# Performance work log

Measured on AMD Instinct MI355X. Metric: run time of the kernel, lower is better.

Reference implementation:

```python
import jax, jax.numpy as jnp
import numpy as np

D_MODEL = 512
N_HEADS = 8
HEAD_DIM = D_MODEL // N_HEADS
SEQ = 2048
BATCH = 2
EPS = 1e-5
SCALE = 1.0 / np.sqrt(HEAD_DIM).astype(np.float32)
# (kind, window, dilation) per head, matching init_kwargs head_specs
SPECS = [("global", 0, 1), ("global", 0, 1),
         ("window", 64, 1), ("window", 128, 1), ("window", 256, 1),
         ("dilated", 64, 2), ("dilated", 64, 4), ("dilated", 64, 8)]


def build_masks(N):
    i = jnp.arange(N)
    D = jnp.abs(i[:, None] - i[None, :])
    ms = []
    for kind, w, dil in SPECS:
        if kind == "global":
            ms.append(jnp.ones((N, N), dtype=bool))
        elif kind == "window":
            ms.append(D <= w)
        else:  # dilated
            ms.append((D % dil == 0) & (D // dil <= w))
    return jnp.stack(ms)  # [H, N, N] bool


def layernorm(x, g, b):
    mu = jnp.mean(x, axis=-1, keepdims=True)
    var = jnp.mean((x - mu) ** 2, axis=-1, keepdims=True)
    return (x - mu) * jax.lax.rsqrt(var + EPS) * g + b


def setup_inputs() -> dict:
    key = jax.random.key(0)
    ks = jax.random.split(key, 7)
    w = 0.02
    return {
        "x": jax.random.normal(ks[0], (BATCH, SEQ, D_MODEL), dtype=jnp.float32),
        "Wq": jax.random.normal(ks[1], (D_MODEL, D_MODEL), dtype=jnp.float32) * w,
        "Wk": jax.random.normal(ks[2], (D_MODEL, D_MODEL), dtype=jnp.float32) * w,
        "Wv": jax.random.normal(ks[3], (D_MODEL, D_MODEL), dtype=jnp.float32) * w,
        "Wo": jax.random.normal(ks[4], (D_MODEL, D_MODEL), dtype=jnp.float32) * w,
        "T_w1": jax.random.normal(ks[5], (D_MODEL, D_MODEL), dtype=jnp.float32) * w,
        "T_b1": jnp.zeros((D_MODEL,), dtype=jnp.float32),
        "T_w2": jax.random.normal(ks[6], (1, D_MODEL), dtype=jnp.float32) * w,
        "T_b2": jnp.zeros((1,), dtype=jnp.float32),
        "ln_in_g": jnp.ones((D_MODEL,), dtype=jnp.float32),
        "ln_in_b": jnp.zeros((D_MODEL,), dtype=jnp.float32),
        "ln_out_g": jnp.ones((D_MODEL,), dtype=jnp.float32),
        "ln_out_b": jnp.zeros((D_MODEL,), dtype=jnp.float32),
    }


def reference(x, Wq, Wk, Wv, Wo, T_w1, T_b1, T_w2, T_b2,
              ln_in_g, ln_in_b, ln_out_g, ln_out_b):
    B, N, H = x.shape
    x0 = x
    xn = layernorm(x, ln_in_g, ln_in_b)
    # torch Linear: y = x @ W.T ; reshape to [B, h, N, d]
    def heads(W):
        return (xn @ W.T).reshape(B, N, N_HEADS, HEAD_DIM).transpose(0, 2, 1, 3)
    Q, K, V = heads(Wq), heads(Wk), heads(Wv)
    attn = jnp.einsum("bhqd,bhkd->bhqk", Q, K) * SCALE
    mask = build_masks(N)  # [h, N, N]
    attn = jnp.where(mask[None], attn, -jnp.inf)
    attn = jax.nn.softmax(attn, axis=-1)  # every row has diagonal unmasked
    out = jnp.einsum("bhqk,bhkd->bhqd", attn, V)
    out = out.transpose(0, 2, 1, 3).reshape(B, N, N_HEADS * HEAD_DIM)
    out = out @ Wo.T
    # tanh-gated softmax over sequence dim
    T_logits = jnp.tanh(xn @ T_w1.T + T_b1) @ T_w2.T + T_b2  # [B, N, 1]
    T = jax.nn.softmax(T_logits, axis=1)
    out = out * T
    return layernorm(out + x0, ln_out_g, ln_out_b)
```

## Files before the change

### kernel.cpp

```cpp
#include <hip/hip_runtime.h>
#include <math.h>

#define N_SEQ 2048
#define DM    512
#define NTOK  4096
#define NH    8
#define HD    64
#define NSLOT 25
#define CHUNK 5

typedef __attribute__((ext_vector_type(8))) short short8;
typedef __attribute__((ext_vector_type(4))) short short4_t;
typedef __attribute__((ext_vector_type(4))) float f32x4;

__device__ inline short f2bf(float x) {
    union { float f; unsigned u; } v; v.f = x;
    unsigned r = v.u + 0x7fff + ((v.u >> 16) & 1);
    return (short)(r >> 16);
}
__device__ inline float bf2f(short s) {
    union { unsigned u; float f; } v; v.u = ((unsigned)(unsigned short)s) << 16;
    return v.f;
}
__device__ inline unsigned pkbf(float a, float b) {
    return ((unsigned)(unsigned short)f2bf(b) << 16) | (unsigned)(unsigned short)f2bf(a);
}
__device__ inline float ftanh(float x) {
    float e = __expf(2.f * x);
    return 1.f - 2.f / (e + 1.f);
}

__device__ inline f32x4 mfma16(short8 a, short8 b, f32x4 c) {
    return __builtin_amdgcn_mfma_f32_16x16x32_bf16(a, b, c, 0, 0, 0);
}

__device__ __forceinline__ void async_cp16(const short* g, short* l) {
    __builtin_amdgcn_global_load_lds(
        (const __attribute__((address_space(1))) void*)g,
        (__attribute__((address_space(3))) void*)l, 16, 0, 0);
}

__global__ __launch_bounds__(128) void k_ln(const float* __restrict__ x,
                                            const float* __restrict__ g,
                                            const float* __restrict__ b,
                                            short* __restrict__ y,
                                            float* __restrict__ lg) {
    int tk = blockIdx.x, t = threadIdx.x;
    if (t == 0) lg[tk] = 0.f;
    float4 xv = ((const float4*)(x + (size_t)tk * DM))[t];
    float s = xv.x + xv.y + xv.z + xv.w;
    float q = xv.x*xv.x + xv.y*xv.y + xv.z*xv.z + xv.w*xv.w;
    for (int o = 32; o; o >>= 1) { s += __shfl_down(s, o); q += __shfl_down(q, o); }
    __shared__ float ls[2], lq[2];
    if ((t & 63) == 0) { ls[t >> 6] = s; lq[t >> 6] = q; }
    __syncthreads();
    s = ls[0] + ls[1]; q = lq[0] + lq[1];
    float mu = s * (1.f / DM);
    float var = q * (1.f / DM) - mu * mu;
    float rs = rsqrtf(var + 1e-5f);
    float4 gv = ((const float4*)g)[t], bv = ((const float4*)b)[t];
    short4_t o;
    o[0] = f2bf((xv.x - mu) * rs * gv.x + bv.x);
    o[1] = f2bf((xv.y - mu) * rs * gv.y + bv.y);
    o[2] = f2bf((xv.z - mu) * rs * gv.z + bv.z);
    o[3] = f2bf((xv.w - mu) * rs * gv.w + bv.w);
    *(short4_t*)&y[(size_t)tk * DM + t * 4] = o;
}

__global__ __launch_bounds__(256) void k_cvtw(
    const float* __restrict__ Wq, const float* __restrict__ Wk,
    const float* __restrict__ Wv, const float* __restrict__ Tw1,
    const float* __restrict__ Wo,
    short* __restrict__ wcat, short* __restrict__ wo) {
    int id = blockIdx.x * 256 + threadIdx.x;
    if (id < 262144) {
        int z = id >> 16; int off = id & 65535;
        const float* s = (z == 0) ? Wq : (z == 1) ? Wk : (z == 2) ? Wv : Tw1;
        float4 v = ((const float4*)s)[off];
        short4_t o = {f2bf(v.x), f2bf(v.y), f2bf(v.z), f2bf(v.w)};
        *(short4_t*)(wcat + (size_t)z * 262144 + (size_t)off * 4) = o;
    } else {
        int off = id - 262144;
        float4 v = ((const float4*)Wo)[off];
        short4_t o = {f2bf(v.x), f2bf(v.y), f2bf(v.z), f2bf(v.w)};
        *(short4_t*)(wo + (size_t)off * 4) = o;
    }
}

__global__ __launch_bounds__(256) void k_gemm(
    const short* __restrict__ A, const short* __restrict__ W, int qkvt,
    const float* __restrict__ Tb1, const float* __restrict__ Tw2,
    short* __restrict__ qb, short* __restrict__ kb, short* __restrict__ vb,
    float* __restrict__ lg, float* __restrict__ proj) {
    __shared__ short As[128 * 32];
    __shared__ short Bs[128 * 32];
    int t = threadIdx.x;
    int lane = t & 63, w = t >> 6;
    int wy = w >> 1, wx = w & 1;
    int ln = lane & 15, q4 = lane >> 4;
    int c0 = blockIdx.x * 128, m0 = blockIdx.y * 128;
    int sr = t >> 2, sc = (t & 3) << 3;
    f32x4 acc[4][4];
    f32x4 zero = {0.f, 0.f, 0.f, 0.f};
    #pragma unroll
    for (int i = 0; i < 4; i++)
        #pragma unroll
        for (int j = 0; j < 4; j++) acc[i][j] = zero;
    for (int k0 = 0; k0 < DM; k0 += 32) {
        __syncthreads();
        async_cp16(&A[(size_t)(m0 + sr) * DM + k0 + sc],      &As[sr * 32 + sc]);
        async_cp16(&A[(size_t)(m0 + 64 + sr) * DM + k0 + sc], &As[(64 + sr) * 32 + sc]);
        async_cp16(&W[(size_t)(c0 + sr) * DM + k0 + sc],      &Bs[sr * 32 + sc]);
        async_cp16(&W[(size_t)(c0 + 64 + sr) * DM + k0 + sc], &Bs[(64 + sr) * 32 + sc]);
        __syncthreads();
        short8 af[4], bfr[4];
        #pragma unroll
        for (int i = 0; i < 4; i++)
            af[i] = *(short8*)&As[(wy * 64 + i * 16 + ln) * 32 + q4 * 8];
        #pragma unroll
        for (int j = 0; j < 4; j++)
            bfr[j] = *(short8*)&Bs[(wx * 64 + j * 16 + ln) * 32 + q4 * 8];
        #pragma unroll
        for (int i = 0; i < 4; i++)
            #pragma unroll
            for (int j = 0; j < 4; j++)
                acc[i][j] = mfma16(af[i], bfr[j], acc[i][j]);
    }
    if (qkvt) {
        int z = c0 >> 9;
        if (z < 3) {
            short* dst = (z == 0) ? qb : (z == 1) ? kb : vb;
            float sc2 = (z == 0) ? 0.125f : 1.0f;
            #pragma unroll
            for (int i = 0; i < 4; i++)
                #pragma unroll
                for (int j = 0; j < 4; j++)
                    #pragma unroll
                    for (int r = 0; r < 4; r++) {
                        int row = m0 + wy * 64 + i * 16 + q4 * 4 + r;
                        int col = c0 + wx * 64 + j * 16 + ln;
                        int nin = col & 511;
                        int h = nin >> 6, d = nin & 63;
                        int bi = row >> 11, n = row & (N_SEQ - 1);
                        dst[(((size_t)bi * NH + h) * N_SEQ + n) * HD + d] =
                            f2bf(acc[i][j][r] * sc2);
                    }
        } else {
            #pragma unroll
            for (int i = 0; i < 4; i++) {
                #pragma unroll
                for (int r = 0; r < 4; r++) {
                    float s = 0.f;
                    #pragma unroll
                    for (int j = 0; j < 4; j++) {
                        int tc = (c0 & 511) + wx * 64 + j * 16 + ln;
                        s += ftanh(acc[i][j][r] + Tb1[tc]) * Tw2[tc];
                    }
                    s += __shfl_xor(s, 1);
                    s += __shfl_xor(s, 2);
                    s += __shfl_xor(s, 4);
                    s += __shfl_xor(s, 8);
                    if (ln == 0) {
                        int row = m0 + wy * 64 + i * 16 + q4 * 4 + r;
                        atomicAdd(&lg[row], s);
                    }
                }
            }
        }
    } else {
        #pragma unroll
        for (int i = 0; i < 4; i++)
            #pragma unroll
            for (int j = 0; j < 4; j++)
                #pragma unroll
                for (int r = 0; r < 4; r++) {
                    int row = m0 + wy * 64 + i * 16 + q4 * 4 + r;
                    int col = c0 + wx * 64 + j * 16 + ln;
                    proj[(size_t)row * DM + col] = acc[i][j][r];
                }
    }
}

__global__ __launch_bounds__(256) void k_vtr(const short* __restrict__ vb,
                                             short* __restrict__ vtb) {
    __shared__ short tile[64][80];
    int t = threadIdx.x;
    int n0 = blockIdx.x * 64, bh = blockIdx.y;
    const short* src = vb + (size_t)bh * N_SEQ * HD;
    short* dst = vtb + (size_t)bh * HD * N_SEQ;
    #pragma unroll
    for (int i = 0; i < 2; i++) {
        int id = t + 256 * i;
        int r = id >> 3, c = id & 7;
        *(short8*)&tile[r][c * 8] = *(const short8*)&src[(size_t)(n0 + r) * HD + c * 8];
    }
    __syncthreads();
    #pragma unroll
    for (int i = 0; i < 2; i++) {
        int id = t + 256 * i;
        int d = id >> 3, c = id & 7;
        short8 v;
        #pragma unroll
        for (int j = 0; j < 8; j++) v[j] = tile[c * 8 + j][d];
        *(short8*)&dst[(size_t)d * N_SEQ + n0 + c * 8] = v;
    }
}

__global__ __launch_bounds__(1024) void k_gate(const float* __restrict__ lg,
                                               float* __restrict__ gate) {
    int b = blockIdx.x, t = threadIdx.x;
    __shared__ float red[16];
    float v0 = lg[b * N_SEQ + t], v1 = lg[b * N_SEQ + 1024 + t];
    float m = fmaxf(v0, v1);
    for (int o = 32; o; o >>= 1) m = fmaxf(m, __shfl_down(m, o));
    if ((t & 63) == 0) red[t >> 6] = m;
    __syncthreads();
    if (t < 64) {
        float x = (t < 16) ? red[t] : -INFINITY;
        for (int o = 8; o; o >>= 1) x = fmaxf(x, __shfl_down(x, o));
        if (t == 0) red[0] = x;
    }
    __syncthreads();
    float M = red[0];
    float e0 = __expf(v0 - M), e1 = __expf(v1 - M);
    float s = e0 + e1;
    __syncthreads();
    for (int o = 32; o; o >>= 1) s += __shfl_down(s, o);
    if ((t & 63) == 0) red[t >> 6] = s;
    __syncthreads();
    if (t < 64) {
        float x = (t < 16) ? red[t] : 0.f;
        for (int o = 8; o; o >>= 1) x += __shfl_down(x, o);
        if (t == 0) red[0] = x;
    }
    __syncthreads();
    float inv = 1.f / red[0];
    gate[b * N_SEQ + t] = e0 * inv;
    gate[b * N_SEQ + 1024 + t] = e1 * inv;
}

__global__ __launch_bounds__(256) void k_attn(const short* __restrict__ qb,
                                              const short* __restrict__ kb,
                                              const short* __restrict__ vtb,
                                              short* __restrict__ P_O,
                                              float* __restrict__ P_ml) {
    __shared__ short Ks[64 * 72];
    __shared__ short Vt[64 * 72];
    __shared__ short Pa[4][16 * 72];
    int t = threadIdx.x;
    int lane = t & 63, w = t >> 6;
    int ln = lane & 15, q4 = lane >> 4;
    int slot = blockIdx.x, qt = blockIdx.y, bi = blockIdx.z;
    int q0 = qt * 64;
    int h, c;
    if (slot < 7)        { h = 0; c = slot; }
    else if (slot < 14)  { h = 1; c = slot - 7; }
    else if (slot == 14) { h = 2; c = 0; }
    else if (slot == 15) { h = 3; c = 0; }
    else if (slot < 18)  { h = 4; c = slot - 16; }
    else if (slot == 18) { h = 5; c = 0; }
    else if (slot < 21)  { h = 6; c = slot - 19; }
    else                 { h = 7; c = slot - 21; }
    int kind = (h < 2) ? 0 : (h < 5) ? 1 : 2;
    int wnd = (h == 2 || h >= 5) ? 64 : (h == 3) ? 128 : (h == 4) ? 256 : 0;
    int dsh = (h == 5) ? 1 : (h == 6) ? 2 : (h == 7) ? 3 : 0;
    int dmask = (1 << dsh) - 1;
    int wmax = (kind == 0) ? 0 : (wnd << dsh);
    int tLoU, tHiU;
    if (kind == 0) { tLoU = 0; tHiU = 31; }
    else { tLoU = (q0 - wmax) >> 6; tHiU = (q0 + 63 + wmax) >> 6; }
    int ktLo = tLoU + c * CHUNK;
    int ktHi = ktLo + CHUNK - 1;
    if (ktHi > tHiU) ktHi = tHiU;
    if (ktHi > 31) ktHi = 31;
    if (ktLo < 0) ktLo = 0;
    int p4 = (bi * 32 + qt) * NSLOT + slot;
    float* ml = P_ml + (size_t)p4 * 128;
    if (ktLo > ktHi) {
        if (t < 64) { ml[t] = -1e30f; ml[64 + t] = 0.f; }
        return;
    }
    const size_t base = ((size_t)bi * NH + h) * N_SEQ * HD;
    const short* Q = qb + base;
    const short* K = kb + base;
    const short* Vg = vtb + base;
    short8 qa[2];
    {
        const short* qrow = Q + (size_t)(q0 + w * 16 + ln) * HD + q4 * 8;
        qa[0] = *(const short8*)qrow;
        qa[1] = *(const short8*)(qrow + 32);
    }
    int qi = q0 + w * 16 + ln;
    float m_i = -1e30f, l_i = 0.f;
    f32x4 OT[4];
    f32x4 zero = {0.f, 0.f, 0.f, 0.f};
    #pragma unroll
    for (int d = 0; d < 4; d++) OT[d] = zero;
    short* Paw = Pa[w];
    for (int kt = ktLo; kt <= ktHi; kt++) {
        int k0 = kt << 6;
        __syncthreads();
        #pragma unroll
        for (int i2 = 0; i2 < 2; i2++) {
            int id = t + 256 * i2;
            int r = id >> 3, cc = id & 7;
            *(short8*)&Ks[r * 72 + cc * 8] =
                *(const short8*)&K[(size_t)(k0 + r) * HD + cc * 8];
            *(short8*)&Vt[r * 72 + cc * 8] =
                *(const short8*)&Vg[(size_t)r * N_SEQ + k0 + cc * 8];
        }
        __syncthreads();
        f32x4 ST[4];
        #pragma unroll
        for (int nt = 0; nt < 4; nt++) ST[nt] = zero;
        #pragma unroll
        for (int nt = 0; nt < 4; nt++) {
            #pragma unroll
            for (int ks = 0; ks < 2; ks++) {
                short8 af = *(short8*)&Ks[(nt * 16 + ln) * 72 + ks * 32 + q4 * 8];
                ST[nt] = mfma16(af, qa[ks], ST[nt]);
            }
        }
        if (kind != 0) {
            #pragma unroll
            for (int nt = 0; nt < 4; nt++)
                #pragma unroll
                for (int r = 0; r < 4; r++) {
                    int key = k0 + nt * 16 + q4 * 4 + r;
                    int dlt = qi - key; dlt = (dlt < 0) ? -dlt : dlt;
                    int valid;
                    if (kind == 1) valid = (dlt <= wnd);
                    else valid = ((dlt & dmask) == 0) && ((dlt >> dsh) <= wnd);
                    if (!valid) ST[nt][r] = -1e30f;
                }
        }
        float rm = -1e30f;
        #pragma unroll
        for (int nt = 0; nt < 4; nt++) {
            float a = fmaxf(ST[nt][0], ST[nt][1]);
            float b = fmaxf(ST[nt][2], ST[nt][3]);
            rm = fmaxf(rm, fmaxf(a, b));
        }
        rm = fmaxf(rm, __shfl_xor(rm, 16));
        rm = fmaxf(rm, __shfl_xor(rm, 32));
        float mn = fmaxf(m_i, rm);
        float sc = __expf(m_i - mn);
        float rs = 0.f;
        #pragma unroll
        for (int nt = 0; nt < 4; nt++) {
            float p0 = __expf(ST[nt][0] - mn);
            float p1 = __expf(ST[nt][1] - mn);
            float p2 = __expf(ST[nt][2] - mn);
            float p3 = __expf(ST[nt][3] - mn);
            rs += (p0 + p1) + (p2 + p3);
            *(unsigned*)&Paw[ln * 72 + nt * 16 + q4 * 4]     = pkbf(p0, p1);
            *(unsigned*)&Paw[ln * 72 + nt * 16 + q4 * 4 + 2] = pkbf(p2, p3);
        }
        rs += __shfl_xor(rs, 16);
        rs += __shfl_xor(rs, 32);
        l_i = l_i * sc + rs;
        m_i = mn;
        #pragma unroll
        for (int d = 0; d < 4; d++) OT[d] *= sc;
        short8 pb0 = *(short8*)&Paw[ln * 72 + q4 * 8];
        short8 pb1 = *(short8*)&Paw[ln * 72 + 32 + q4 * 8];
        #pragma unroll
        for (int dt = 0; dt < 4; dt++) {
            short8 a0 = *(short8*)&Vt[(dt * 16 + ln) * 72 + q4 * 8];
            short8 a1 = *(short8*)&Vt[(dt * 16 + ln) * 72 + 32 + q4 * 8];
            OT[dt] = mfma16(a0, pb0, OT[dt]);
            OT[dt] = mfma16(a1, pb1, OT[dt]);
        }
    }
    if (q4 == 0) { ml[w * 16 + ln] = m_i; ml[64 + w * 16 + ln] = l_i; }
    #pragma unroll
    for (int dt = 0; dt < 4; dt++) {
        *(unsigned*)&Paw[ln * 72 + dt * 16 + q4 * 4]     = pkbf(OT[dt][0], OT[dt][1]);
        *(unsigned*)&Paw[ln * 72 + dt * 16 + q4 * 4 + 2] = pkbf(OT[dt][2], OT[dt][3]);
    }
    short8 o0 = *(short8*)&Paw[ln * 72 + q4 * 16];
    short8 o1 = *(short8*)&Paw[ln * 72 + q4 * 16 + 8];
    short* Op = P_O + (size_t)p4 * 4096;
    *(short8*)&Op[(w * 16 + ln) * 64 + q4 * 16] = o0;
    *(short8*)&Op[(w * 16 + ln) * 64 + q4 * 16 + 8] = o1;
}

__global__ __launch_bounds__(256) void k_combine(const short* __restrict__ P_O,
                                                 const float* __restrict__ P_ml,
                                                 short* __restrict__ ob) {
    const int hbase[8] = {0, 7, 14, 15, 16, 18, 19, 21};
    const int hcnt[8]  = {7, 7, 1, 1, 2, 1, 2, 4};
    int h = blockIdx.x, qt = blockIdx.y, bi = blockIdx.z;
    int t = threadIdx.x;
    int row = t >> 2, c0 = (t & 3) * 16;
    int pb = (bi * 32 + qt) * NSLOT + hbase[h];
    int cnt = hcnt[h];
    float m = -1e30f;
    for (int s = 0; s < cnt; s++)
        m = fmaxf(m, P_ml[(size_t)(pb + s) * 128 + row]);
    float l = 0.f;
    float acc[16];
    #pragma unroll
    for (int j = 0; j < 16; j++) acc[j] = 0.f;
    for (int s = 0; s < cnt; s++) {
        float ms = P_ml[(size_t)(pb + s) * 128 + row];
        float ls = P_ml[(size_t)(pb + s) * 128 + 64 + row];
        if (ls > 0.f) {
            float sc = __expf(ms - m);
            l += ls * sc;
            const short* Op = P_O + (size_t)(pb + s) * 4096 + row * 64 + c0;
            short8 v0 = *(const short8*)Op;
            short8 v1 = *(const short8*)(Op + 8);
            #pragma unroll
            for (int j = 0; j < 8; j++) acc[j]     += bf2f(v0[j]) * sc;
            #pragma unroll
            for (int j = 0; j < 8; j++) acc[8 + j] += bf2f(v1[j]) * sc;
        }
    }
    float inv = 1.f / l;
    int n = qt * 64 + row;
    short8 o0, o1;
    #pragma unroll
    for (int j = 0; j < 8; j++) o0[j] = f2bf(acc[j] * inv);
    #pragma unroll
    for (int j = 0; j < 8; j++) o1[j] = f2bf(acc[8 + j] * inv);
    short* dst = ob + ((size_t)bi * N_SEQ + n) * DM + h * 64 + c0;
    *(short8*)dst = o0;
    *(short8*)(dst + 8) = o1;
}

__global__ __launch_bounds__(128) void k_final(const float* __restrict__ proj,
                                               const float* __restrict__ gate,
                                               const float* __restrict__ x0,
                                               const float* __restrict__ g,
                                               const float* __restrict__ b,
                                               float* __restrict__ out) {
    int tk = blockIdx.x, t = threadIdx.x;
    float gt = gate[tk];
    float4 pv = ((const float4*)(proj + (size_t)tk * DM))[t];
    float4 xv = ((const float4*)(x0 + (size_t)tk * DM))[t];
    float4 y;
    y.x = pv.x * gt + xv.x;
    y.y = pv.y * gt + xv.y;
    y.z = pv.z * gt + xv.z;
    y.w = pv.w * gt + xv.w;
    float s = y.x + y.y + y.z + y.w;
    float q = y.x*y.x + y.y*y.y + y.z*y.z + y.w*y.w;
    for (int o = 32; o; o >>= 1) { s += __shfl_down(s, o); q += __shfl_down(q, o); }
    __shared__ float ls[2], lq[2];
    if ((t & 63) == 0) { ls[t >> 6] = s; lq[t >> 6] = q; }
    __syncthreads();
    s = ls[0] + ls[1]; q = lq[0] + lq[1];
    float mu = s * (1.f / DM);
    float var = q * (1.f / DM) - mu * mu;
    float rs = rsqrtf(var + 1e-5f);
    float4 gv = ((const float4*)g)[t], bv = ((const float4*)b)[t];
    float4 o;
    o.x = (y.x - mu) * rs * gv.x + bv.x;
    o.y = (y.y - mu) * rs * gv.y + bv.y;
    o.z = (y.z - mu) * rs * gv.z + bv.z;
    o.w = (y.w - mu) * rs * gv.w + bv.w;
    ((float4*)(out + (size_t)tk * DM))[t] = o;
}

extern "C" void kernel_launch(void* const* d_in, const int* in_sizes, int n_in,
                              void* d_out, int out_size, void* d_ws, size_t ws_size,
                              hipStream_t stream) {
    (void)in_sizes; (void)n_in; (void)out_size; (void)ws_size;
    const float* x    = (const float*)d_in[0];
    const float* Wq   = (const float*)d_in[1];
    const float* Wk   = (const float*)d_in[2];
    const float* Wv   = (const float*)d_in[3];
    const float* Wo   = (const float*)d_in[4];
    const float* Tw1  = (const float*)d_in[5];
    const float* Tb1  = (const float*)d_in[6];
    const float* Tw2  = (const float*)d_in[7];
    const float* ling = (const float*)d_in[9];
    const float* linb = (const float*)d_in[10];
    const float* logg = (const float*)d_in[11];
    const float* logb = (const float*)d_in[12];
    float* out = (float*)d_out;

    const size_t SZ = (size_t)NTOK * DM;
    const int NPART = 2 * 32 * NSLOT;
    char* p = (char*)d_ws;
    short* xn   = (short*)p; p += SZ * 2;
    short* wcat = (short*)p; p += (size_t)2048 * DM * 2;
    short* wo   = (short*)p; p += (size_t)DM * DM * 2;
    short* qb   = (short*)p; p += SZ * 2;
    short* kb   = (short*)p; p += SZ * 2;
    short* vb   = (short*)p; p += SZ * 2;
    short* vtb  = (short*)p; p += SZ * 2;
    short* obuf = (short*)p; p += SZ * 2;
    float* lg   = (float*)p; p += (size_t)NTOK * 4;
    float* gate = (float*)p; p += (size_t)NTOK * 4;
    float* P_ml = (float*)p; p += (size_t)NPART * 128 * 4;
    float* proj = (float*)p;
    short* P_O  = (short*)p; p += (size_t)NPART * 4096 * 2;

    k_ln<<<NTOK, 128, 0, stream>>>(x, ling, linb, xn, lg);
    k_cvtw<<<1280, 256, 0, stream>>>(Wq, Wk, Wv, Tw1, Wo, wcat, wo);
    k_gemm<<<dim3(16, 32), 256, 0, stream>>>(xn, wcat, 1, Tb1, Tw2,
                                             qb, kb, vb, lg, nullptr);
    k_vtr<<<dim3(32, 16), 256, 0, stream>>>(vb, vtb);
    k_gate<<<2, 1024, 0, stream>>>(lg, gate);
    k_attn<<<dim3(NSLOT, 32, 2), 256, 0, stream>>>(qb, kb, vtb, P_O, P_ml);
    k_combine<<<dim3(8, 32, 2), 256, 0, stream>>>(P_O, P_ml, obuf);
    k_gemm<<<dim3(4, 32), 256, 0, stream>>>(obuf, wo, 0, nullptr, nullptr,
                                            nullptr, nullptr, nullptr, nullptr, proj);
    k_final<<<NTOK, 128, 0, stream>>>(proj, gate, x, logg, logb, out);
}
```

Baseline: 173.9 us.

## Merge small kernels, widen attention key tiles to 128, split output GEMM finer

Folds layernorm and weight conversion into one launch, and V transpose and gate softmax into another. The QKV/T GEMM and the output projection GEMM become separate kernels, and the output projection now uses 64-wide column tiles so it launches twice as many blocks. The attention kernel processes 128 keys per iteration instead of 64 and uses fewer partition slots (18 instead of 25), with the combine tables updated to match. The aim is to cut launch overhead and per-tile loop and sync overhead, at the cost of more LDS per attention block and less parallelism across slots.

```diff
diff --git a/kernel.cpp b/kernel.cpp
--- a/kernel.cpp
+++ b/kernel.cpp
@@ -6,8 +6,7 @@
 #define NTOK  4096
 #define NH    8
 #define HD    64
-#define NSLOT 25
-#define CHUNK 5
+#define NSLOT 18
 
 typedef __attribute__((ext_vector_type(8))) short short8;
 typedef __attribute__((ext_vector_type(4))) short short4_t;
@@ -40,58 +39,59 @@
         (__attribute__((address_space(3))) void*)l, 16, 0, 0);
 }
 
-__global__ __launch_bounds__(128) void k_ln(const float* __restrict__ x,
-                                            const float* __restrict__ g,
-                                            const float* __restrict__ b,
-                                            short* __restrict__ y,
-                                            float* __restrict__ lg) {
-    int tk = blockIdx.x, t = threadIdx.x;
-    if (t == 0) lg[tk] = 0.f;
-    float4 xv = ((const float4*)(x + (size_t)tk * DM))[t];
-    float s = xv.x + xv.y + xv.z + xv.w;
-    float q = xv.x*xv.x + xv.y*xv.y + xv.z*xv.z + xv.w*xv.w;
-    for (int o = 32; o; o >>= 1) { s += __shfl_down(s, o); q += __shfl_down(q, o); }
-    __shared__ float ls[2], lq[2];
-    if ((t & 63) == 0) { ls[t >> 6] = s; lq[t >> 6] = q; }
-    __syncthreads();
-    s = ls[0] + ls[1]; q = lq[0] + lq[1];
-    float mu = s * (1.f / DM);
-    float var = q * (1.f / DM) - mu * mu;
-    float rs = rsqrtf(var + 1e-5f);
-    float4 gv = ((const float4*)g)[t], bv = ((const float4*)b)[t];
-    short4_t o;
-    o[0] = f2bf((xv.x - mu) * rs * gv.x + bv.x);
-    o[1] = f2bf((xv.y - mu) * rs * gv.y + bv.y);
-    o[2] = f2bf((xv.z - mu) * rs * gv.z + bv.z);
-    o[3] = f2bf((xv.w - mu) * rs * gv.w + bv.w);
-    *(short4_t*)&y[(size_t)tk * DM + t * 4] = o;
-}
-
-__global__ __launch_bounds__(256) void k_cvtw(
+__global__ __launch_bounds__(256) void k_lncvt(
+    const float* __restrict__ x, const float* __restrict__ g,
+    const float* __restrict__ b, short* __restrict__ y, float* __restrict__ lg,
     const float* __restrict__ Wq, const float* __restrict__ Wk,
     const float* __restrict__ Wv, const float* __restrict__ Tw1,
     const float* __restrict__ Wo,
     short* __restrict__ wcat, short* __restrict__ wo) {
-    int id = blockIdx.x * 256 + threadIdx.x;
-    if (id < 262144) {
-        int z = id >> 16; int off = id & 65535;
-        const float* s = (z == 0) ? Wq : (z == 1) ? Wk : (z == 2) ? Wv : Tw1;
-        float4 v = ((const float4*)s)[off];
-        short4_t o = {f2bf(v.x), f2bf(v.y), f2bf(v.z), f2bf(v.w)};
-        *(short4_t*)(wcat + (size_t)z * 262144 + (size_t)off * 4) = o;
+    int blk = blockIdx.x, t = threadIdx.x;
+    if (blk < 2048) {
+        int sub = t >> 7, tt = t & 127;
+        int tk = blk * 2 + sub;
+        if (tt == 0) lg[tk] = 0.f;
+        float4 xv = ((const float4*)(x + (size_t)tk * DM))[tt];
+        float s = xv.x + xv.y + xv.z + xv.w;
+        float q = xv.x*xv.x + xv.y*xv.y + xv.z*xv.z + xv.w*xv.w;
+        for (int o = 32; o; o >>= 1) { s += __shfl_down(s, o); q += __shfl_down(q, o); }
+        __shared__ float ls[4], lq[4];
+        if ((t & 63) == 0) { ls[t >> 6] = s; lq[t >> 6] = q; }
+        __syncthreads();
+        s = ls[sub * 2] + ls[sub * 2 + 1];
+        q = lq[sub * 2] + lq[sub * 2 + 1];
+        float mu = s * (1.f / DM);
+        float var = q * (1.f / DM) - mu * mu;
+        float rs = rsqrtf(var + 1e-5f);
+        float4 gv = ((const float4*)g)[tt], bv = ((const float4*)b)[tt];
+        short4_t o;
+        o[0] = f2bf((xv.x - mu) * rs * gv.x + bv.x);
+        o[1] = f2bf((xv.y - mu) * rs * gv.y + bv.y);
+        o[2] = f2bf((xv.z - mu) * rs * gv.z + bv.z);
+        o[3] = f2bf((xv.w - mu) * rs * gv.w + bv.w);
+        *(short4_t*)&y[(size_t)tk * DM + tt * 4] = o;
     } else {
-        int off = id - 262144;
-        float4 v = ((const float4*)Wo)[off];
-        short4_t o = {f2bf(v.x), f2bf(v.y), f2bf(v.z), f2bf(v.w)};
-        *(short4_t*)(wo + (size_t)off * 4) = o;
-    }
-}
-
-__global__ __launch_bounds__(256) void k_gemm(
-    const short* __restrict__ A, const short* __restrict__ W, int qkvt,
+        int id = (blk - 2048) * 256 + t;
+        if (id < 262144) {
+            int z = id >> 16; int off = id & 65535;
+            const float* s = (z == 0) ? Wq : (z == 1) ? Wk : (z == 2) ? Wv : Tw1;
+            float4 v = ((const float4*)s)[off];
+            short4_t o = {f2bf(v.x), f2bf(v.y), f2bf(v.z), f2bf(v.w)};
+            *(short4_t*)(wcat + (size_t)z * 262144 + (size_t)off * 4) = o;
+        } else {
+            int off = id - 262144;
+            float4 v = ((const float4*)Wo)[off];
+            short4_t o = {f2bf(v.x), f2bf(v.y), f2bf(v.z), f2bf(v.w)};
+            *(short4_t*)(wo + (size_t)off * 4) = o;
+        }
+    }
+}
+
+__global__ __launch_bounds__(256) void k_gemmqkvt(
+    const short* __restrict__ A, const short* __restrict__ W,
     const float* __restrict__ Tb1, const float* __restrict__ Tw2,
     short* __restrict__ qb, short* __restrict__ kb, short* __restrict__ vb,
-    float* __restrict__ lg, float* __restrict__ proj) {
+    float* __restrict__ lg) {
     __shared__ short As[128 * 32];
     __shared__ short Bs[128 * 32];
     int t = threadIdx.x;
@@ -126,48 +126,10 @@
             for (int j = 0; j < 4; j++)
                 acc[i][j] = mfma16(af[i], bfr[j], acc[i][j]);
     }
-    if (qkvt) {
-        int z = c0 >> 9;
-        if (z < 3) {
-            short* dst = (z == 0) ? qb : (z == 1) ? kb : vb;
-            float sc2 = (z == 0) ? 0.125f : 1.0f;
-            #pragma unroll
-            for (int i = 0; i < 4; i++)
-                #pragma unroll
-                for (int j = 0; j < 4; j++)
-                    #pragma unroll
-                    for (int r = 0; r < 4; r++) {
-                        int row = m0 + wy * 64 + i * 16 + q4 * 4 + r;
-                        int col = c0 + wx * 64 + j * 16 + ln;
-                        int nin = col & 511;
-                        int h = nin >> 6, d = nin & 63;
-                        int bi = row >> 11, n = row & (N_SEQ - 1);
-                        dst[(((size_t)bi * NH + h) * N_SEQ + n) * HD + d] =
-                            f2bf(acc[i][j][r] * sc2);
-                    }
-        } else {
-            #pragma unroll
-            for (int i = 0; i < 4; i++) {
-                #pragma unroll
-                for (int r = 0; r < 4; r++) {
-                    float s = 0.f;
-                    #pragma unroll
-                    for (int j = 0; j < 4; j++) {
-                        int tc = (c0 & 511) + wx * 64 + j * 16 + ln;
-                        s += ftanh(acc[i][j][r] + Tb1[tc]) * Tw2[tc];
-                    }
-                    s += __shfl_xor(s, 1);
-                    s += __shfl_xor(s, 2);
-                    s += __shfl_xor(s, 4);
-                    s += __shfl_xor(s, 8);
-                    if (ln == 0) {
-                        int row = m0 + wy * 64 + i * 16 + q4 * 4 + r;
-                        atomicAdd(&lg[row], s);
-                    }
-                }
-            }
-        }
-    } else {
+    int z = c0 >> 9;
+    if (z < 3) {
+        short* dst = (z == 0) ? qb : (z == 1) ? kb : vb;
+        float sc2 = (z == 0) ? 0.125f : 1.0f;
         #pragma unroll
         for (int i = 0; i < 4; i++)
             #pragma unroll
@@ -176,67 +138,140 @@
                 for (int r = 0; r < 4; r++) {
                     int row = m0 + wy * 64 + i * 16 + q4 * 4 + r;
                     int col = c0 + wx * 64 + j * 16 + ln;
-                    proj[(size_t)row * DM + col] = acc[i][j][r];
+                    int nin = col & 511;
+                    int h = nin >> 6, d = nin & 63;
+                    int bi = row >> 11, n = row & (N_SEQ - 1);
+                    dst[(((size_t)bi * NH + h) * N_SEQ + n) * HD + d] =
+                        f2bf(acc[i][j][r] * sc2);
                 }
-    }
-}
-
-__global__ __launch_bounds__(256) void k_vtr(const short* __restrict__ vb,
-                                             short* __restrict__ vtb) {
+    } else {
+        #pragma unroll
+        for (int i = 0; i < 4; i++) {
+            #pragma unroll
+            for (int r = 0; r < 4; r++) {
+                float s = 0.f;
+                #pragma unroll
+                for (int j = 0; j < 4; j++) {
+                    int tc = (c0 & 511) + wx * 64 + j * 16 + ln;
+                    s += ftanh(acc[i][j][r] + Tb1[tc]) * Tw2[tc];
+                }
+                s += __shfl_xor(s, 1);
+                s += __shfl_xor(s, 2);
+                s += __shfl_xor(s, 4);
+                s += __shfl_xor(s, 8);
+                if (ln == 0) {
+                    int row = m0 + wy * 64 + i * 16 + q4 * 4 + r;
+                    atomicAdd(&lg[row], s);
+                }
+            }
+        }
+    }
+}
+
+__global__ __launch_bounds__(256) void k_gemmp(
+    const short* __restrict__ A, const short* __restrict__ W,
+    float* __restrict__ proj) {
+    __shared__ short As[128 * 32];
+    __shared__ short Bs[64 * 32];
+    int t = threadIdx.x;
+    int lane = t & 63, w = t >> 6;
+    int wy = w >> 1, wx = w & 1;
+    int ln = lane & 15, q4 = lane >> 4;
+    int c0 = blockIdx.x * 64, m0 = blockIdx.y * 128;
+    int sr = t >> 2, sc = (t & 3) << 3;
+    int br = t >> 2, bc = (t & 3) << 3;
+    f32x4 acc[4][2];
+    f32x4 zero = {0.f, 0.f, 0.f, 0.f};
+    #pragma unroll
+    for (int i = 0; i < 4; i++) { acc[i][0] = zero; acc[i][1] = zero; }
+    for (int k0 = 0; k0 < DM; k0 += 32) {
+        __syncthreads();
+        async_cp16(&A[(size_t)(m0 + sr) * DM + k0 + sc],      &As[sr * 32 + sc]);
+        async_cp16(&A[(size_t)(m0 + 64 + sr) * DM + k0 + sc], &As[(64 + sr) * 32 + sc]);
+        if (br < 64)
+            async_cp16(&W[(size_t)(c0 + br) * DM + k0 + bc], &Bs[br * 32 + bc]);
+        __syncthreads();
+        short8 af[4], bfr[2];
+        #pragma unroll
+        for (int i = 0; i < 4; i++)
+            af[i] = *(short8*)&As[(wy * 64 + i * 16 + ln) * 32 + q4 * 8];
+        #pragma unroll
+        for (int j = 0; j < 2; j++)
+            bfr[j] = *(short8*)&Bs[(wx * 32 + j * 16 + ln) * 32 + q4 * 8];
+        #pragma unroll
+        for (int i = 0; i < 4; i++)
+            #pragma unroll
+            for (int j = 0; j < 2; j++)
+                acc[i][j] = mfma16(af[i], bfr[j], acc[i][j]);
+    }
+    #pragma unroll
+    for (int i = 0; i < 4; i++)
+        #pragma unroll
+        for (int j = 0; j < 2; j++)
+            #pragma unroll
+            for (int r = 0; r < 4; r++) {
+                int row = m0 + wy * 64 + i * 16 + q4 * 4 + r;
+                int col = c0 + wx * 32 + j * 16 + ln;
+                proj[(size_t)row * DM + col] = acc[i][j][r];
+            }
+}
+
+__global__ __launch_bounds__(256) void k_vtrgate(const short* __restrict__ vb,
+                                                 short* __restrict__ vtb,
+                                                 const float* __restrict__ lg,
+                                                 float* __restrict__ gate) {
     __shared__ short tile[64][80];
-    int t = threadIdx.x;
-    int n0 = blockIdx.x * 64, bh = blockIdx.y;
-    const short* src = vb + (size_t)bh * N_SEQ * HD;
-    short* dst = vtb + (size_t)bh * HD * N_SEQ;
-    #pragma unroll
-    for (int i = 0; i < 2; i++) {
-        int id = t + 256 * i;
-        int r = id >> 3, c = id & 7;
-        *(short8*)&tile[r][c * 8] = *(const short8*)&src[(size_t)(n0 + r) * HD + c * 8];
-    }
-    __syncthreads();
-    #pragma unroll
-    for (int i = 0; i < 2; i++) {
-        int id = t + 256 * i;
-        int d = id >> 3, c = id & 7;
-        short8 v;
-        #pragma unroll
-        for (int j = 0; j < 8; j++) v[j] = tile[c * 8 + j][d];
-        *(short8*)&dst[(size_t)d * N_SEQ + n0 + c * 8] = v;
-    }
-}
-
-__global__ __launch_bounds__(1024) void k_gate(const float* __restrict__ lg,
-                                               float* __restrict__ gate) {
-    int b = blockIdx.x, t = threadIdx.x;
-    __shared__ float red[16];
-    float v0 = lg[b * N_SEQ + t], v1 = lg[b * N_SEQ + 1024 + t];
-    float m = fmaxf(v0, v1);
-    for (int o = 32; o; o >>= 1) m = fmaxf(m, __shfl_down(m, o));
-    if ((t & 63) == 0) red[t >> 6] = m;
-    __syncthreads();
-    if (t < 64) {
-        float x = (t < 16) ? red[t] : -INFINITY;
-        for (int o = 8; o; o >>= 1) x = fmaxf(x, __shfl_down(x, o));
-        if (t == 0) red[0] = x;
-    }
-    __syncthreads();
-    float M = red[0];
-    float e0 = __expf(v0 - M), e1 = __expf(v1 - M);
-    float s = e0 + e1;
-    __syncthreads();
-    for (int o = 32; o; o >>= 1) s += __shfl_down(s, o);
-    if ((t & 63) == 0) red[t >> 6] = s;
-    __syncthreads();
-    if (t < 64) {
-        float x = (t < 16) ? red[t] : 0.f;
-        for (int o = 8; o; o >>= 1) x += __shfl_down(x, o);
-        if (t == 0) red[0] = x;
-    }
-    __syncthreads();
-    float inv = 1.f / red[0];
-    gate[b * N_SEQ + t] = e0 * inv;
-    gate[b * N_SEQ + 1024 + t] = e1 * inv;
+    __shared__ float rg[8];
+    int blk = blockIdx.x, t = threadIdx.x;
+    if (blk < 512) {
+        int n0 = (blk & 31) * 64, bh = blk >> 5;
+        const short* src = vb + (size_t)bh * N_SEQ * HD;
+        short* dst = vtb + (size_t)bh * HD * N_SEQ;
+        #pragma unroll
+        for (int i = 0; i < 2; i++) {
+            int id = t + 256 * i;
+            int r = id >> 3, c = id & 7;
+            *(short8*)&tile[r][c * 8] = *(const short8*)&src[(size_t)(n0 + r) * HD + c * 8];
+        }
+        __syncthreads();
+        #pragma unroll
+        for (int i = 0; i < 2; i++) {
+            int id = t + 256 * i;
+            int d = id >> 3, c = id & 7;
+            short8 v;
+            #pragma unroll
+            for (int j = 0; j < 8; j++) v[j] = tile[c * 8 + j][d];
+            *(short8*)&dst[(size_t)d * N_SEQ + n0 + c * 8] = v;
+        }
+    } else {
+        int b = blk - 512;
+        float v[8];
+        {
+            float4 a0 = *(const float4*)&lg[b * N_SEQ + t * 8];
+            float4 a1 = *(const float4*)&lg[b * N_SEQ + t * 8 + 4];
+            v[0] = a0.x; v[1] = a0.y; v[2] = a0.z; v[3] = a0.w;
+            v[4] = a1.x; v[5] = a1.y; v[6] = a1.z; v[7] = a1.w;
+        }
+        float m = v[0];
+        #pragma unroll
+        for (int j = 1; j < 8; j++) m = fmaxf(m, v[j]);
+        for (int o = 32; o; o >>= 1) m = fmaxf(m, __shfl_down(m, o));
+        if ((t & 63) == 0) rg[t >> 6] = m;
+        __syncthreads();
+        m = fmaxf(fmaxf(rg[0], rg[1]), fmaxf(rg[2], rg[3]));
+        float e[8], s = 0.f;
+        #pragma unroll
+        for (int j = 0; j < 8; j++) { e[j] = __expf(v[j] - m); s += e[j]; }
+        for (int o = 32; o; o >>= 1) s += __shfl_down(s, o);
+        if ((t & 63) == 0) rg[4 + (t >> 6)] = s;
+        __syncthreads();
+        s = (rg[4] + rg[5]) + (rg[6] + rg[7]);
+        float inv = 1.f / s;
+        float4 o0 = {e[0] * inv, e[1] * inv, e[2] * inv, e[3] * inv};
+        float4 o1 = {e[4] * inv, e[5] * inv, e[6] * inv, e[7] * inv};
+        *(float4*)&gate[b * N_SEQ + t * 8] = o0;
+        *(float4*)&gate[b * N_SEQ + t * 8 + 4] = o1;
+    }
 }
 
 __global__ __launch_bounds__(256) void k_attn(const short* __restrict__ qb,
@@ -244,35 +279,35 @@
                                               const short* __restrict__ vtb,
                                               short* __restrict__ P_O,
                                               float* __restrict__ P_ml) {
-    __shared__ short Ks[64 * 72];
-    __shared__ short Vt[64 * 72];
-    __shared__ short Pa[4][16 * 72];
+    __shared__ short Ks[128 * 72];
+    __shared__ short Vt[64 * 136];
+    __shared__ short Pa[4][16 * 136];
     int t = threadIdx.x;
     int lane = t & 63, w = t >> 6;
     int ln = lane & 15, q4 = lane >> 4;
     int slot = blockIdx.x, qt = blockIdx.y, bi = blockIdx.z;
     int q0 = qt * 64;
     int h, c;
-    if (slot < 7)        { h = 0; c = slot; }
-    else if (slot < 14)  { h = 1; c = slot - 7; }
-    else if (slot == 14) { h = 2; c = 0; }
-    else if (slot == 15) { h = 3; c = 0; }
-    else if (slot < 18)  { h = 4; c = slot - 16; }
-    else if (slot == 18) { h = 5; c = 0; }
-    else if (slot < 21)  { h = 6; c = slot - 19; }
-    else                 { h = 7; c = slot - 21; }
+    if (slot < 4)        { h = 0; c = slot; }
+    else if (slot < 8)   { h = 1; c = slot - 4; }
+    else if (slot == 8)  { h = 2; c = 0; }
+    else if (slot == 9)  { h = 3; c = 0; }
+    else if (slot < 12)  { h = 4; c = slot - 10; }
+    else if (slot == 12) { h = 5; c = 0; }
+    else if (slot < 15)  { h = 6; c = slot - 13; }
+    else                 { h = 7; c = slot - 15; }
     int kind = (h < 2) ? 0 : (h < 5) ? 1 : 2;
     int wnd = (h == 2 || h >= 5) ? 64 : (h == 3) ? 128 : (h == 4) ? 256 : 0;
     int dsh = (h == 5) ? 1 : (h == 6) ? 2 : (h == 7) ? 3 : 0;
     int dmask = (1 << dsh) - 1;
     int wmax = (kind == 0) ? 0 : (wnd << dsh);
-    int tLoU, tHiU;
-    if (kind == 0) { tLoU = 0; tHiU = 31; }
-    else { tLoU = (q0 - wmax) >> 6; tHiU = (q0 + 63 + wmax) >> 6; }
-    int ktLo = tLoU + c * CHUNK;
-    int ktHi = ktLo + CHUNK - 1;
+    int tLoU, tHiU, CS;
+    if (kind == 0) { tLoU = 0; tHiU = 15; CS = 4; }
+    else { tLoU = (q0 - wmax) >> 7; tHiU = (q0 + 63 + wmax) >> 7; CS = 3; }
+    int ktLo = tLoU + c * CS;
+    int ktHi = ktLo + CS - 1;
     if (ktHi > tHiU) ktHi = tHiU;
-    if (ktHi > 31) ktHi = 31;
+    if (ktHi > 15) ktHi = 15;
     if (ktLo < 0) ktLo = 0;
     int p4 = (bi * 32 + qt) * NSLOT + slot;
     float* ml = P_ml + (size_t)p4 * 128;
@@ -298,23 +333,24 @@
     for (int d = 0; d < 4; d++) OT[d] = zero;
     short* Paw = Pa[w];
     for (int kt = ktLo; kt <= ktHi; kt++) {
-        int k0 = kt << 6;
-        __syncthreads();
-        #pragma unroll
-        for (int i2 = 0; i2 < 2; i2++) {
+        int k0 = kt << 7;
+        __syncthreads();
+        #pragma unroll
+        for (int i2 = 0; i2 < 4; i2++) {
             int id = t + 256 * i2;
-            int r = id >> 3, cc = id & 7;
-            *(short8*)&Ks[r * 72 + cc * 8] =
-                *(const short8*)&K[(size_t)(k0 + r) * HD + cc * 8];
-            *(short8*)&Vt[r * 72 + cc * 8] =
-                *(const short8*)&Vg[(size_t)r * N_SEQ + k0 + cc * 8];
-        }
-        __syncthreads();
-        f32x4 ST[4];
-        #pragma unroll
-        for (int nt = 0; nt < 4; nt++) ST[nt] = zero;
-        #pragma unroll
-        for (int nt = 0; nt < 4; nt++) {
+            int kr = id >> 3, cc = id & 7;
+            *(short8*)&Ks[kr * 72 + cc * 8] =
+                *(const short8*)&K[(size_t)(k0 + kr) * HD + cc * 8];
+            int dr = id >> 4, kc = id & 15;
+            *(short8*)&Vt[dr * 136 + kc * 8] =
+                *(const short8*)&Vg[(size_t)dr * N_SEQ + k0 + kc * 8];
+        }
+        __syncthreads();
+        f32x4 ST[8];
+        #pragma unroll
+        for (int nt = 0; nt < 8; nt++) ST[nt] = zero;
+        #pragma unroll
+        for (int nt = 0; nt < 8; nt++) {
             #pragma unroll
             for (int ks = 0; ks < 2; ks++) {
                 short8 af = *(short8*)&Ks[(nt * 16 + ln) * 72 + ks * 32 + q4 * 8];
@@ -323,7 +359,7 @@
         }
         if (kind != 0) {
             #pragma unroll
-            for (int nt = 0; nt < 4; nt++)
+            for (int nt = 0; nt < 8; nt++)
                 #pragma unroll
                 for (int r = 0; r < 4; r++) {
                     int key = k0 + nt * 16 + q4 * 4 + r;
@@ -336,7 +372,7 @@
         }
         float rm = -1e30f;
         #pragma unroll
-        for (int nt = 0; nt < 4; nt++) {
+        for (int nt = 0; nt < 8; nt++) {
             float a = fmaxf(ST[nt][0], ST[nt][1]);
             float b = fmaxf(ST[nt][2], ST[nt][3]);
             rm = fmaxf(rm, fmaxf(a, b));
@@ -347,14 +383,14 @@
         float sc = __expf(m_i - mn);
         float rs = 0.f;
         #pragma unroll
-        for (int nt = 0; nt < 4; nt++) {
+        for (int nt = 0; nt < 8; nt++) {
             float p0 = __expf(ST[nt][0] - mn);
             float p1 = __expf(ST[nt][1] - mn);
             float p2 = __expf(ST[nt][2] - mn);
             float p3 = __expf(ST[nt][3] - mn);
             rs += (p0 + p1) + (p2 + p3);
-            *(unsigned*)&Paw[ln * 72 + nt * 16 + q4 * 4]     = pkbf(p0, p1);
-            *(unsigned*)&Paw[ln * 72 + nt * 16 + q4 * 4 + 2] = pkbf(p2, p3);
+            *(unsigned*)&Paw[ln * 136 + nt * 16 + q4 * 4]     = pkbf(p0, p1);
+            *(unsigned*)&Paw[ln * 136 + nt * 16 + q4 * 4 + 2] = pkbf(p2, p3);
         }
         rs += __shfl_xor(rs, 16);
         rs += __shfl_xor(rs, 32);
@@ -362,24 +398,27 @@
         m_i = mn;
         #pragma unroll
         for (int d = 0; d < 4; d++) OT[d] *= sc;
-        short8 pb0 = *(short8*)&Paw[ln * 72 + q4 * 8];
-        short8 pb1 = *(short8*)&Paw[ln * 72 + 32 + q4 * 8];
+        short8 pb[4];
+        #pragma unroll
+        for (int ks = 0; ks < 4; ks++)
+            pb[ks] = *(short8*)&Paw[ln * 136 + ks * 32 + q4 * 8];
         #pragma unroll
         for (int dt = 0; dt < 4; dt++) {
-            short8 a0 = *(short8*)&Vt[(dt * 16 + ln) * 72 + q4 * 8];
-            short8 a1 = *(short8*)&Vt[(dt * 16 + ln) * 72 + 32 + q4 * 8];
-            OT[dt] = mfma16(a0, pb0, OT[dt]);
-            OT[dt] = mfma16(a1, pb1, OT[dt]);
+            #pragma unroll
+            for (int ks = 0; ks < 4; ks++) {
+                short8 a = *(short8*)&Vt[(dt * 16 + ln) * 136 + ks * 32 + q4 * 8];
+                OT[dt] = mfma16(a, pb[ks], OT[dt]);
+            }
         }
     }
     if (q4 == 0) { ml[w * 16 + ln] = m_i; ml[64 + w * 16 + ln] = l_i; }
     #pragma unroll
     for (int dt = 0; dt < 4; dt++) {
-        *(unsigned*)&Paw[ln * 72 + dt * 16 + q4 * 4]     = pkbf(OT[dt][0], OT[dt][1]);
-        *(unsigned*)&Paw[ln * 72 + dt * 16 + q4 * 4 + 2] = pkbf(OT[dt][2], OT[dt][3]);
-    }
-    short8 o0 = *(short8*)&Paw[ln * 72 + q4 * 16];
-    short8 o1 = *(short8*)&Paw[ln * 72 + q4 * 16 + 8];
+        *(unsigned*)&Paw[ln * 136 + dt * 16 + q4 * 4]     = pkbf(OT[dt][0], OT[dt][1]);
+        *(unsigned*)&Paw[ln * 136 + dt * 16 + q4 * 4 + 2] = pkbf(OT[dt][2], OT[dt][3]);
+    }
+    short8 o0 = *(short8*)&Paw[ln * 136 + q4 * 16];
+    short8 o1 = *(short8*)&Paw[ln * 136 + q4 * 16 + 8];
     short* Op = P_O + (size_t)p4 * 4096;
     *(short8*)&Op[(w * 16 + ln) * 64 + q4 * 16] = o0;
     *(short8*)&Op[(w * 16 + ln) * 64 + q4 * 16 + 8] = o1;
@@ -388,8 +427,8 @@
 __global__ __launch_bounds__(256) void k_combine(const short* __restrict__ P_O,
                                                  const float* __restrict__ P_ml,
                                                  short* __restrict__ ob) {
-    const int hbase[8] = {0, 7, 14, 15, 16, 18, 19, 21};
-    const int hcnt[8]  = {7, 7, 1, 1, 2, 1, 2, 4};
+    const int hbase[8] = {0, 4, 8, 9, 10, 12, 13, 15};
+    const int hcnt[8]  = {4, 4, 1, 1, 2, 1, 2, 3};
     int h = blockIdx.x, qt = blockIdx.y, bi = blockIdx.z;
     int t = threadIdx.x;
     int row = t >> 2, c0 = (t & 3) * 16;
@@ -498,15 +537,13 @@
     float* proj = (float*)p;
     short* P_O  = (short*)p; p += (size_t)NPART * 4096 * 2;
 
-    k_ln<<<NTOK, 128, 0, stream>>>(x, ling, linb, xn, lg);
-    k_cvtw<<<1280, 256, 0, stream>>>(Wq, Wk, Wv, Tw1, Wo, wcat, wo);
-    k_gemm<<<dim3(16, 32), 256, 0, stream>>>(xn, wcat, 1, Tb1, Tw2,
-                                             qb, kb, vb, lg, nullptr);
-    k_vtr<<<dim3(32, 16), 256, 0, stream>>>(vb, vtb);
-    k_gate<<<2, 1024, 0, stream>>>(lg, gate);
+    k_lncvt<<<3328, 256, 0, stream>>>(x, ling, linb, xn, lg,
+                                      Wq, Wk, Wv, Tw1, Wo, wcat, wo);
+    k_gemmqkvt<<<dim3(16, 32), 256, 0, stream>>>(xn, wcat, Tb1, Tw2,
+                                                 qb, kb, vb, lg);
+    k_vtrgate<<<514, 256, 0, stream>>>(vb, vtb, lg, gate);
     k_attn<<<dim3(NSLOT, 32, 2), 256, 0, stream>>>(qb, kb, vtb, P_O, P_ml);
     k_combine<<<dim3(8, 32, 2), 256, 0, stream>>>(P_O, P_ml, obuf);
-    k_gemm<<<dim3(4, 32), 256, 0, stream>>>(obuf, wo, 0, nullptr, nullptr,
-                                            nullptr, nullptr, nullptr, nullptr, proj);
+    k_gemmp<<<dim3(8, 32), 256, 0, stream>>>(obuf, wo, proj);
     k_final<<<NTOK, 128, 0, stream>>>(proj, gate, x, logg, logb, out);
 }
```

Result: faster. 161.8 us (-6.9%).
